# Performance work log

Hardware: AMD Instinct MI355X
Metric: run time of the kernel (lower is better)

## Reference

```python
import jax, jax.numpy as jnp
import numpy as np

T, B, IN, H = 512, 64, 1024, 1024

def setup_inputs() -> dict:
    key = jax.random.key(0)
    ks = jax.random.split(key, 7)
    X = jax.random.normal(ks[0], (T, B, IN), dtype=jnp.float32)
    h0 = jax.random.normal(ks[1], (B, H), dtype=jnp.float32)
    c0 = jax.random.normal(ks[2], (B, H), dtype=jnp.float32)
    mask = jax.random.randint(ks[3], (T, B), 0, 2, dtype=jnp.int32)
    # orthogonal-ish init approximated with scaled normal (math is identical at runtime)
    W_x_ifoc = jax.random.normal(ks[4], (4 * H, IN), dtype=jnp.float32) / np.sqrt(IN)
    W_h_ifoc = jax.random.normal(ks[5], (4 * H, H), dtype=jnp.float32) / np.sqrt(H)
    b_ifoc = jnp.zeros((4 * H,), dtype=jnp.float32)
    return {"X": X, "h0": h0, "c0": c0, "mask": mask,
            "W_x_ifoc": W_x_ifoc, "W_h_ifoc": W_h_ifoc, "b_ifoc": b_ifoc}

def reference(X, h0, c0, mask, W_x_ifoc, W_h_ifoc, b_ifoc):
    Hd = h0.shape[-1]
    # precompute input projection for all timesteps: [T, B, 4H]
    X4 = jnp.einsum('tbi,gi->tbg', X, W_x_ifoc) + b_ifoc
    m_f = mask.astype(X.dtype)[..., None]  # [T, B, 1]

    def step(carry, inp):
        pre_h, pre_c = carry
        x4, m = inp
        # NOTE: recurrent matmul is applied to the CELL state (non-standard)
        pre = x4 + pre_c @ W_h_ifoc.T  # [B, 4H]
        i, f, o, g = jnp.split(pre, 4, axis=-1)
        i = jax.nn.sigmoid(i)
        f = jax.nn.sigmoid(f)
        o = jax.nn.sigmoid(o)
        c = f * pre_c + i * jnp.tanh(g)
        h = o * jnp.tanh(c)
        h = h * m + pre_h * (1 - m)
        c = c * m + pre_c * (1 - m)
        return (h, c), h

    (h_last, c_last), hiddens = jax.lax.scan(step, (h0, c0), (X4, m_f))
    return hiddens, h_last, c_last
```

## Files before the change

kernel.cpp:

```cpp
#include <hip/hip_runtime.h>
#include <cstdint>
#include <cstddef>

#define T_STEPS 512
#define BATCH   64
#define HD      1024
#define BH      (BATCH * HD)
#define NBLK    256
#define NSG     4
#define BSG     16
#define JBLK    16

using half8   = __attribute__((ext_vector_type(8))) _Float16;
using half4   = __attribute__((ext_vector_type(4))) _Float16;
using floatx4 = __attribute__((ext_vector_type(4))) float;
using float4v = __attribute__((ext_vector_type(4))) float;
using u64     = unsigned long long;

__device__ __forceinline__ float sigmoidf_(float x) { return 1.0f / (1.0f + __expf(-x)); }

__device__ __forceinline__ half8 cvt_h8(float4v a, float4v b) {
    half8 r;
    r[0] = (_Float16)a[0]; r[1] = (_Float16)a[1];
    r[2] = (_Float16)a[2]; r[3] = (_Float16)a[3];
    r[4] = (_Float16)b[0]; r[5] = (_Float16)b[1];
    r[6] = (_Float16)b[2]; r[7] = (_Float16)b[3];
    return r;
}

__device__ __forceinline__ void st_sc1_b64(_Float16* p, u64 v) {
    asm volatile("global_store_dwordx2 %0, %1, off sc0 sc1"
                 :: "v"(p), "v"(v) : "memory");
}

__device__ __forceinline__ u64 pack_lo16(unsigned a, unsigned b, unsigned c, unsigned d) {
    return (u64)(a & 0xffffu) | ((u64)(b & 0xffffu) << 16)
         | ((u64)(c & 0xffffu) << 32) | ((u64)(d & 0xffffu) << 48);
}
__device__ __forceinline__ u64 pack_hi16(unsigned a, unsigned b, unsigned c, unsigned d) {
    return (u64)(a >> 16) | ((u64)(b >> 16) << 16)
         | ((u64)(c >> 16) << 32) | ((u64)(d >> 16) << 48);
}

static const size_t BAR_GRP_OFF  = 0;
static const size_t BAR_ROOT_OFF = 20480;
static const size_t CH_OFF  = 24576;
static const size_t CL_OFF  = CH_OFF + (size_t)2 * BH * 2;
static const size_t WX_OFF  = 1u << 20;
static const size_t WHH_OFF = WX_OFF  + (size_t)8 * 1024 * 1024;
static const size_t WHL_OFF = WHH_OFF + (size_t)8 * 1024 * 1024;
static const size_t XH_OFF  = WHL_OFF + (size_t)8 * 1024 * 1024;
static const size_t X4_OFF  = XH_OFF;
static const size_t TIER_A2_WS = X4_OFF + (size_t)32768 * 4096 * 2;
static const size_t TIER_A_WS  = XH_OFF + (size_t)T_STEPS * BH * 2;
static const size_t TIER_B_WS  = XH_OFF;

__global__ void prep_zero(int* bar) {
    int i = blockIdx.x * 256 + threadIdx.x;
    if (i < 6144) bar[i] = 0;
}

__global__ void prep_w(const float* __restrict__ Wx, const float* __restrict__ Wh,
                       _Float16* __restrict__ wx16,
                       _Float16* __restrict__ whh, _Float16* __restrict__ whl) {
    int i = blockIdx.x * 256 + threadIdx.x;
    if (i < 4 * HD * HD) {
        wx16[i] = (_Float16)Wx[i];
        float w = Wh[i];
        _Float16 h = (_Float16)w;
        whh[i] = h;
        whl[i] = (_Float16)(w - (float)h);
    }
}

__global__ void prep_x(const float* __restrict__ X, _Float16* __restrict__ xh) {
    size_t i = (size_t)blockIdx.x * 256 + threadIdx.x;
    if (i < (size_t)T_STEPS * BH) xh[i] = (_Float16)X[i];
}

__global__ __launch_bounds__(256) void x4_gemm(
    const float* __restrict__ X,
    const _Float16* __restrict__ wx16,
    _Float16* __restrict__ x4)
{
    __shared__ _Float16 sA[128][40];
    __shared__ _Float16 sB[128][40];

    const int tid  = threadIdx.x;
    const int wave = tid >> 6;
    const int lane = tid & 63;
    const int m0 = blockIdx.x * 128, n0 = blockIdx.y * 128;
    const int wm = (wave & 1) * 64,  wn = (wave >> 1) * 64;
    const int fm = lane & 15, q = lane >> 4;

    floatx4 acc[4][4];
    #pragma unroll
    for (int i = 0; i < 4; i++)
        #pragma unroll
        for (int j = 0; j < 4; j++)
            acc[i][j] = (floatx4){0.f, 0.f, 0.f, 0.f};

    for (int k0 = 0; k0 < 1024; k0 += 32) {
        {
            const int kq = (tid & 7) * 4;
            const int rb = tid >> 3;
            #pragma unroll
            for (int it = 0; it < 4; it++) {
                int row = rb + it * 32;
                float4v v = *(const float4v*)(X + (size_t)(m0 + row) * 1024 + k0 + kq);
                half4 h; h[0] = (_Float16)v[0]; h[1] = (_Float16)v[1];
                h[2] = (_Float16)v[2]; h[3] = (_Float16)v[3];
                *(half4*)&sA[row][kq] = h;
            }
        }
        {
            const int half = tid & 1;
            const int row  = tid >> 1;
            const _Float16* src = wx16 + (size_t)(n0 + row) * 1024 + k0 + half * 16;
            *(half8*)&sB[row][half * 16]     = *(const half8*)(src);
            *(half8*)&sB[row][half * 16 + 8] = *(const half8*)(src + 8);
        }
        __syncthreads();

        half8 af[4], bf[4];
        #pragma unroll
        for (int i = 0; i < 4; i++) af[i] = *(const half8*)&sA[wm + 16 * i + fm][q * 8];
        #pragma unroll
        for (int j = 0; j < 4; j++) bf[j] = *(const half8*)&sB[wn + 16 * j + fm][q * 8];
        #pragma unroll
        for (int i = 0; i < 4; i++)
            #pragma unroll
            for (int j = 0; j < 4; j++)
                acc[i][j] = __builtin_amdgcn_mfma_f32_16x16x32_f16(af[i], bf[j], acc[i][j], 0, 0, 0);
        __syncthreads();
    }

    #pragma unroll
    for (int i = 0; i < 4; i++)
        #pragma unroll
        for (int j = 0; j < 4; j++)
            #pragma unroll
            for (int r = 0; r < 4; r++) {
                int row = m0 + wm + 16 * i + q * 4 + r;
                int col = n0 + wn + 16 * j + fm;
                x4[(size_t)row * 4096 + col] = (_Float16)acc[i][j][r];
            }
}

__device__ __forceinline__ void grid_bar(int* grp, int* root, int slot) {
    __syncthreads();
    if (threadIdx.x == 0) {
        int g = blockIdx.x >> 5;
        int v = __hip_atomic_fetch_add(&grp[slot * 8 + g], 1,
                                       __ATOMIC_ACQ_REL, __HIP_MEMORY_SCOPE_AGENT);
        if (v == 31)
            __hip_atomic_fetch_add(&root[slot], 1,
                                   __ATOMIC_ACQ_REL, __HIP_MEMORY_SCOPE_AGENT);
        while (__hip_atomic_load(&root[slot], __ATOMIC_RELAXED,
                                 __HIP_MEMORY_SCOPE_AGENT) < 8)
            __builtin_amdgcn_s_sleep(2);
        (void)__hip_atomic_load(&root[slot], __ATOMIC_ACQUIRE,
                                __HIP_MEMORY_SCOPE_AGENT);
    }
    __syncthreads();
}

__device__ __forceinline__ void gbar(int* grp, int* root, int& bcnt) {
    asm volatile("s_waitcnt vmcnt(0)" ::: "memory");
    __syncthreads();
    bcnt++;
    if (threadIdx.x == 0) {
        int v = __hip_atomic_fetch_add(grp, 1, __ATOMIC_RELAXED, __HIP_MEMORY_SCOPE_AGENT);
        if (v == 8 * bcnt - 1)
            __hip_atomic_fetch_add(root, 1, __ATOMIC_RELAXED, __HIP_MEMORY_SCOPE_AGENT);
        while (__hip_atomic_load(root, __ATOMIC_RELAXED, __HIP_MEMORY_SCOPE_AGENT) < 8 * bcnt)
            __builtin_amdgcn_s_sleep(2);
    }
    __syncthreads();
}

__global__ __launch_bounds__(512, 1) void lstm_persist3(
    const _Float16* __restrict__ x4,
    const float* __restrict__ h0, const float* __restrict__ c0,
    const float* __restrict__ bias, const int* __restrict__ mask,
    const _Float16* __restrict__ whh, const _Float16* __restrict__ whl,
    _Float16* __restrict__ chg, _Float16* __restrict__ clg,
    int* __restrict__ bar,
    float* __restrict__ out)
{
    __shared__ float s_pre[8][4][16][18];
    __shared__ float s_h[256], s_c[256];

    const int tid  = threadIdx.x;
    const int wave = tid >> 6;
    const int lane = tid & 63;
    const int sg   = blockIdx.x >> 6;
    const int lb   = blockIdx.x & 63;
    const int b0   = sg * BSG;
    const int j0   = lb * JBLK;

    int* grp  = bar + (sg * 9 + (lb >> 3)) * 64;
    int* root = bar + (sg * 9 + 8) * 64;
    int  bcnt = 0;

    const int nn    = lane & 15;
    const int q     = lane >> 4;
    const int kbase = wave * 128 + q * 8;
    const int arow  = lane & 15;

    half8 wh_[4][4], wl_[4][4];
    #pragma unroll
    for (int g = 0; g < 4; g++) {
        const size_t wr = (size_t)(g * HD + j0 + nn) * HD + kbase;
        #pragma unroll
        for (int k = 0; k < 4; k++) {
            wh_[g][k] = *(const half8*)(whh + wr + k * 32);
            wl_[g][k] = *(const half8*)(whl + wr + k * 32);
        }
    }

    float biasr[4] = {0.f, 0.f, 0.f, 0.f};
    if (tid < 256) {
        int bl = tid >> 4, n = tid & 15;
        int b = b0 + bl, j = j0 + n;
        float cv = c0[b * HD + j];
        s_c[tid] = cv;
        s_h[tid] = h0[b * HD + j];
        #pragma unroll
        for (int g = 0; g < 4; g++) biasr[g] = bias[g * HD + j];

        _Float16 chi = (_Float16)cv;
        _Float16 clo = (_Float16)(cv - (float)chi);
        unsigned pk = (unsigned)__builtin_bit_cast(unsigned short, chi)
                    | ((unsigned)__builtin_bit_cast(unsigned short, clo) << 16);
        unsigned p1 = __shfl_down(pk, 1);
        unsigned p2 = __shfl_down(pk, 2);
        unsigned p3 = __shfl_down(pk, 3);
        if ((n & 3) == 0) {
            st_sc1_b64(chg + b * HD + j0 + (n & ~3), pack_lo16(pk, p1, p2, p3));
            st_sc1_b64(clg + b * HD + j0 + (n & ~3), pack_hi16(pk, p1, p2, p3));
        }
    }
    gbar(grp, root, bcnt);

    for (int t = 0; t < T_STEPS; t++) {
        const int cur = t & 1;

        float xg[4] = {0.f, 0.f, 0.f, 0.f};
        int   mv    = 0;
        if (tid < 256) {
            int b = b0 + (tid >> 4), j = j0 + (tid & 15);
            #pragma unroll
            for (int g = 0; g < 4; g++)
                xg[g] = (float)x4[((size_t)t * BATCH + b) * 4096 + g * HD + j];
            mv = mask[t * BATCH + b];
        }

        const _Float16* chp = chg + (size_t)cur * BH + (size_t)(b0 + arow) * HD + kbase;
        const _Float16* clp = clg + (size_t)cur * BH + (size_t)(b0 + arow) * HD + kbase;

        half8 a0, a1, a2, a3, l0, l1, l2, l3;
        asm volatile(
            "global_load_dwordx4 %0, %8, off sc0 sc1\n\t"
            "global_load_dwordx4 %1, %8, off offset:64 sc0 sc1\n\t"
            "global_load_dwordx4 %2, %8, off offset:128 sc0 sc1\n\t"
            "global_load_dwordx4 %3, %8, off offset:192 sc0 sc1\n\t"
            "global_load_dwordx4 %4, %9, off sc0 sc1\n\t"
            "global_load_dwordx4 %5, %9, off offset:64 sc0 sc1\n\t"
            "global_load_dwordx4 %6, %9, off offset:128 sc0 sc1\n\t"
            "global_load_dwordx4 %7, %9, off offset:192 sc0 sc1\n\t"
            "s_waitcnt vmcnt(0)"
            : "=&v"(a0), "=&v"(a1), "=&v"(a2), "=&v"(a3),
              "=&v"(l0), "=&v"(l1), "=&v"(l2), "=&v"(l3)
            : "v"(chp), "v"(clp)
            : "memory");

        floatx4 acc[4];
        #pragma unroll
        for (int g = 0; g < 4; g++) acc[g] = (floatx4){0.f, 0.f, 0.f, 0.f};
        #pragma unroll
        for (int g = 0; g < 4; g++) {
            floatx4 t0 = acc[g];
            t0 = __builtin_amdgcn_mfma_f32_16x16x32_f16(a0, wh_[g][0], t0, 0, 0, 0);
            t0 = __builtin_amdgcn_mfma_f32_16x16x32_f16(l0, wh_[g][0], t0, 0, 0, 0);
            t0 = __builtin_amdgcn_mfma_f32_16x16x32_f16(a0, wl_[g][0], t0, 0, 0, 0);
            t0 = __builtin_amdgcn_mfma_f32_16x16x32_f16(a1, wh_[g][1], t0, 0, 0, 0);
            t0 = __builtin_amdgcn_mfma_f32_16x16x32_f16(l1, wh_[g][1], t0, 0, 0, 0);
            t0 = __builtin_amdgcn_mfma_f32_16x16x32_f16(a1, wl_[g][1], t0, 0, 0, 0);
            t0 = __builtin_amdgcn_mfma_f32_16x16x32_f16(a2, wh_[g][2], t0, 0, 0, 0);
            t0 = __builtin_amdgcn_mfma_f32_16x16x32_f16(l2, wh_[g][2], t0, 0, 0, 0);
            t0 = __builtin_amdgcn_mfma_f32_16x16x32_f16(a2, wl_[g][2], t0, 0, 0, 0);
            t0 = __builtin_amdgcn_mfma_f32_16x16x32_f16(a3, wh_[g][3], t0, 0, 0, 0);
            t0 = __builtin_amdgcn_mfma_f32_16x16x32_f16(l3, wh_[g][3], t0, 0, 0, 0);
            t0 = __builtin_amdgcn_mfma_f32_16x16x32_f16(a3, wl_[g][3], t0, 0, 0, 0);
            acc[g] = t0;
        }

        #pragma unroll
        for (int g = 0; g < 4; g++) {
            s_pre[wave][g][q * 4 + 0][nn] = acc[g][0];
            s_pre[wave][g][q * 4 + 1][nn] = acc[g][1];
            s_pre[wave][g][q * 4 + 2][nn] = acc[g][2];
            s_pre[wave][g][q * 4 + 3][nn] = acc[g][3];
        }
        __syncthreads();

        if (tid < 256) {
            int bl = tid >> 4, n = tid & 15;
            int b = b0 + bl, j = j0 + n;

            float pg[4];
            #pragma unroll
            for (int g = 0; g < 4; g++) {
                float s = xg[g] + biasr[g];
                #pragma unroll
                for (int kh = 0; kh < 8; kh++)
                    s += s_pre[kh][g][bl][n];
                pg[g] = s;
            }

            float c_old = s_c[tid];
            float i_g = sigmoidf_(pg[0]);
            float f_g = sigmoidf_(pg[1]);
            float o_g = sigmoidf_(pg[2]);
            float g_g = tanhf(pg[3]);
            float c_new = f_g * c_old + i_g * g_g;
            float h_new = o_g * tanhf(c_new);

            float h_out = mv ? h_new : s_h[tid];
            float c_out = mv ? c_new : c_old;
            s_h[tid] = h_out;
            s_c[tid] = c_out;

            out[(size_t)t * BH + (size_t)b * HD + j] = h_out;

            _Float16 chi = (_Float16)c_out;
            _Float16 clo = (_Float16)(c_out - (float)chi);
            unsigned pk = (unsigned)__builtin_bit_cast(unsigned short, chi)
                        | ((unsigned)__builtin_bit_cast(unsigned short, clo) << 16);
            unsigned p1 = __shfl_down(pk, 1);
            unsigned p2 = __shfl_down(pk, 2);
            unsigned p3 = __shfl_down(pk, 3);
            if ((n & 3) == 0) {
                int nxt = cur ^ 1;
                st_sc1_b64(chg + (size_t)nxt * BH + (size_t)b * HD + j0 + (n & ~3),
                           pack_lo16(pk, p1, p2, p3));
                st_sc1_b64(clg + (size_t)nxt * BH + (size_t)b * HD + j0 + (n & ~3),
                           pack_hi16(pk, p1, p2, p3));
            }

            if (t == T_STEPS - 1) {
                size_t tail = (size_t)T_STEPS * BH;
                out[tail + (size_t)b * HD + j]      = h_out;
                out[tail + BH + (size_t)b * HD + j] = c_out;
            }
        }
        gbar(grp, root, bcnt);
    }
}

template<bool XF16>
__global__ __launch_bounds__(1024, 4) void lstm_persist(
    const float* __restrict__ X, const _Float16* __restrict__ xh,
    const float* __restrict__ h0, const float* __restrict__ c0,
    const float* __restrict__ bias, const int* __restrict__ mask,
    const _Float16* __restrict__ wx16, const _Float16* __restrict__ whh,
    const _Float16* __restrict__ whl,
    _Float16* __restrict__ chg, _Float16* __restrict__ clg,
    int* __restrict__ barg, int* __restrict__ barr,
    float* __restrict__ out)
{
    __shared__ _Float16 s_wh[16 * 1032];
    __shared__ float    s_pre[16][16][17];
    __shared__ float    s_h[256], s_c[256];

    const int tid  = threadIdx.x;
    const int wave = tid >> 6;
    const int lane = tid & 63;
    const int j0   = blockIdx.x * 4;

    for (int idx = tid; idx < 2048; idx += 1024) {
        int n  = idx >> 7;
        int kk = (idx & 127) << 3;
        int r  = (n >> 2) * HD + j0 + (n & 3);
        *(half8*)&s_wh[n * 1032 + kk] = *(const half8*)(whh + (size_t)r * HD + kk);
    }

    float biasr[4] = {0.f, 0.f, 0.f, 0.f};
    if (tid < 256) {
        int b = tid >> 2, jj = tid & 3, j = j0 + jj;
        float cv = c0[b * HD + j];
        s_c[tid] = cv;
        s_h[tid] = h0[b * HD + j];
        _Float16 hi = (_Float16)cv;
        chg[b * HD + j] = hi;
        clg[b * HD + j] = (_Float16)(cv - (float)hi);
        #pragma unroll
        for (int g = 0; g < 4; g++) biasr[g] = bias[g * HD + j];
    }
    grid_bar(barg, barr, 0);

    const int mt    = wave & 3;
    const int kh    = wave >> 2;
    const int arow  = mt * 16 + (lane & 15);
    const int nn    = lane & 15;
    const int q     = lane >> 4;
    const int kbase = kh * 256 + q * 8;
    const int wrow  = (nn >> 2) * HD + j0 + (nn & 3);

    const _Float16* wxp = wx16 + (size_t)wrow * HD + kbase;
    const _Float16* wlp = whl  + (size_t)wrow * HD + kbase;
    const _Float16* whp = (const _Float16*)&s_wh[nn * 1032 + kbase];

    for (int t = 0; t < T_STEPS; t++) {
        const int cur = t & 1;
        const _Float16* chp = chg + (size_t)cur * BH + (size_t)arow * HD + kbase;
        const _Float16* clp = clg + (size_t)cur * BH + (size_t)arow * HD + kbase;

        floatx4 acc = {0.f, 0.f, 0.f, 0.f};

        if (XF16) {
            const _Float16* xp = xh + (size_t)t * BH + (size_t)arow * HD + kbase;
            #pragma unroll 4
            for (int k = 0; k < 256; k += 32) {
                half8 av = *(const half8*)(xp + k);
                half8 bv = *(const half8*)(wxp + k);
                acc = __builtin_amdgcn_mfma_f32_16x16x32_f16(av, bv, acc, 0, 0, 0);
            }
        } else {
            const float* xp = X + (size_t)t * BH + (size_t)arow * HD + kbase;
            #pragma unroll 4
            for (int k = 0; k < 256; k += 32) {
                float4v x0 = *(const float4v*)(xp + k);
                float4v x1 = *(const float4v*)(xp + k + 4);
                half8 av = cvt_h8(x0, x1);
                half8 bv = *(const half8*)(wxp + k);
                acc = __builtin_amdgcn_mfma_f32_16x16x32_f16(av, bv, acc, 0, 0, 0);
            }
        }

        #pragma unroll 4
        for (int k = 0; k < 256; k += 32) {
            half8 ah = *(const half8*)(chp + k);
            half8 al = *(const half8*)(clp + k);
            half8 bh = *(const half8*)(whp + k);
            half8 bl = *(const half8*)(wlp + k);
            acc = __builtin_amdgcn_mfma_f32_16x16x32_f16(ah, bh, acc, 0, 0, 0);
            acc = __builtin_amdgcn_mfma_f32_16x16x32_f16(al, bh, acc, 0, 0, 0);
            acc = __builtin_amdgcn_mfma_f32_16x16x32_f16(ah, bl, acc, 0, 0, 0);
        }

        s_pre[wave][q * 4 + 0][nn] = acc[0];
        s_pre[wave][q * 4 + 1][nn] = acc[1];
        s_pre[wave][q * 4 + 2][nn] = acc[2];
        s_pre[wave][q * 4 + 3][nn] = acc[3];
        __syncthreads();

        if (tid < 256) {
            int b = tid >> 2, jj = tid & 3, j = j0 + jj;
            int m = b & 15, mtt = b >> 4;

            float pg[4];
            #pragma unroll
            for (int g = 0; g < 4; g++) {
                float s = 0.f;
                #pragma unroll
                for (int kk = 0; kk < 4; kk++)
                    s += s_pre[kk * 4 + mtt][m][g * 4 + jj];
                pg[g] = s + biasr[g];
            }

            float c_old = s_c[tid];
            float i_g = sigmoidf_(pg[0]);
            float f_g = sigmoidf_(pg[1]);
            float o_g = sigmoidf_(pg[2]);
            float g_g = tanhf(pg[3]);
            float c_new = f_g * c_old + i_g * g_g;
            float h_new = o_g * tanhf(c_new);

            int mv = mask[t * BATCH + b];
            float h_out = mv ? h_new : s_h[tid];
            float c_out = mv ? c_new : c_old;
            s_h[tid] = h_out;
            s_c[tid] = c_out;

            int nxt = cur ^ 1;
            _Float16 hi = (_Float16)c_out;
            chg[(size_t)nxt * BH + b * HD + j] = hi;
            clg[(size_t)nxt * BH + b * HD + j] = (_Float16)(c_out - (float)hi);
            out[(size_t)t * BH + b * HD + j] = h_out;

            if (t == T_STEPS - 1) {
                size_t tail = (size_t)T_STEPS * BH;
                out[tail + b * HD + j]      = h_out;
                out[tail + BH + b * HD + j] = c_out;
            }
        }
        grid_bar(barg, barr, t + 1);
    }
}

__global__ void init_c_fb(const float* __restrict__ c0, float* __restrict__ cf,
                          _Float16* __restrict__ ch, _Float16* __restrict__ cl) {
    int i = blockIdx.x * 256 + threadIdx.x;
    if (i < BH) {
        float v = c0[i];
        cf[i] = v;
        _Float16 h = (_Float16)v;
        ch[i] = h;
        cl[i] = (_Float16)(v - (float)h);
    }
}

__global__ __launch_bounds__(1024) void lstm_step_fb(
    const float* __restrict__ X, const float* __restrict__ h0,
    const float* __restrict__ Wx, const float* __restrict__ Wh,
    const float* __restrict__ bias, const int* __restrict__ mask,
    float* __restrict__ cf, _Float16* __restrict__ chbuf, _Float16* __restrict__ clbuf,
    float* __restrict__ out, int t)
{
    __shared__ float lds_pre[4][64][16];
    const int tid = threadIdx.x, wave = tid >> 6, lane = tid & 63;
    const int g = wave & 3, mt = wave >> 2, j0 = blockIdx.x * 16;
    const int cur = t & 1;
    const float* cf_prev = cf + (size_t)cur * BH;
    const _Float16* ch_prev = chbuf + (size_t)cur * BH;
    const _Float16* cl_prev = clbuf + (size_t)cur * BH;
    float* cf_next = cf + (size_t)(cur ^ 1) * BH;
    _Float16* ch_next = chbuf + (size_t)(cur ^ 1) * BH;
    _Float16* cl_next = clbuf + (size_t)(cur ^ 1) * BH;
    const int arow = mt * 16 + (lane & 15);
    const int brow = g * HD + j0 + (lane & 15);
    const int koff = (lane >> 4) * 8;
    floatx4 acc = {0.f, 0.f, 0.f, 0.f};
    {
        const float* xp = X + (size_t)t * BH + (size_t)arow * HD + koff;
        const float* wp = Wx + (size_t)brow * HD + koff;
        #pragma unroll 4
        for (int k = 0; k < HD; k += 32) {
            float4v x0 = *(const float4v*)(xp + k);
            float4v x1 = *(const float4v*)(xp + k + 4);
            float4v w0 = *(const float4v*)(wp + k);
            float4v w1 = *(const float4v*)(wp + k + 4);
            acc = __builtin_amdgcn_mfma_f32_16x16x32_f16(cvt_h8(x0, x1), cvt_h8(w0, w1), acc, 0, 0, 0);
        }
    }
    {
        const _Float16* chp = ch_prev + (size_t)arow * HD + koff;
        const _Float16* clp = cl_prev + (size_t)arow * HD + koff;
        const float* whp = Wh + (size_t)brow * HD + koff;
        #pragma unroll 4
        for (int k = 0; k < HD; k += 32) {
            half8 ah = *(const half8*)(chp + k);
            half8 al = *(const half8*)(clp + k);
            float4v w0 = *(const float4v*)(whp + k);
            float4v w1 = *(const float4v*)(whp + k + 4);
            half8 bh = cvt_h8(w0, w1);
            float4v r0, r1;
            r0[0] = w0[0] - (float)bh[0]; r0[1] = w0[1] - (float)bh[1];
            r0[2] = w0[2] - (float)bh[2]; r0[3] = w0[3] - (float)bh[3];
            r1[0] = w1[0] - (float)bh[4]; r1[1] = w1[1] - (float)bh[5];
            r1[2] = w1[2] - (float)bh[6]; r1[3] = w1[3] - (float)bh[7];
            half8 bl = cvt_h8(r0, r1);
            acc = __builtin_amdgcn_mfma_f32_16x16x32_f16(ah, bh, acc, 0, 0, 0);
            acc = __builtin_amdgcn_mfma_f32_16x16x32_f16(al, bh, acc, 0, 0, 0);
            acc = __builtin_amdgcn_mfma_f32_16x16x32_f16(ah, bl, acc, 0, 0, 0);
        }
    }
    {
        const int qq = lane >> 4, col = lane & 15;
        lds_pre[g][mt * 16 + qq * 4 + 0][col] = acc[0];
        lds_pre[g][mt * 16 + qq * 4 + 1][col] = acc[1];
        lds_pre[g][mt * 16 + qq * 4 + 2][col] = acc[2];
        lds_pre[g][mt * 16 + qq * 4 + 3][col] = acc[3];
    }
    __syncthreads();
    {
        const int bl2 = tid >> 4, n = tid & 15, j = j0 + n;
        float pg[4];
        #pragma unroll
        for (int gg = 0; gg < 4; gg++) pg[gg] = lds_pre[gg][bl2][n] + bias[gg * HD + j];
        float c_old = cf_prev[bl2 * HD + j];
        float i_g = sigmoidf_(pg[0]), f_g = sigmoidf_(pg[1]);
        float o_g = sigmoidf_(pg[2]), g_g = tanhf(pg[3]);
        float c_new = f_g * c_old + i_g * g_g;
        float h_new = o_g * tanhf(c_new);
        int mv = mask[t * BATCH + bl2];
        float h_prev = (t == 0) ? h0[bl2 * HD + j] : out[(size_t)(t - 1) * BH + bl2 * HD + j];
        float h_out = mv ? h_new : h_prev;
        float c_out = mv ? c_new : c_old;
        cf_next[bl2 * HD + j] = c_out;
        _Float16 hh = (_Float16)c_out;
        ch_next[bl2 * HD + j] = hh;
        cl_next[bl2 * HD + j] = (_Float16)(c_out - (float)hh);
        out[(size_t)t * BH + bl2 * HD + j] = h_out;
        if (t == T_STEPS - 1) {
            size_t tail = (size_t)T_STEPS * BH;
            out[tail + bl2 * HD + j] = h_out;
            out[tail + BH + bl2 * HD + j] = c_out;
        }
    }
}

extern "C" void kernel_launch(void* const* d_in, const int* in_sizes, int n_in,
                              void* d_out, int out_size, void* d_ws, size_t ws_size,
                              hipStream_t stream) {
    const float* X    = (const float*)d_in[0];
    const float* h0   = (const float*)d_in[1];
    const float* c0   = (const float*)d_in[2];
    const int*   mask = (const int*)  d_in[3];
    const float* Wx   = (const float*)d_in[4];
    const float* Wh   = (const float*)d_in[5];
    const float* bias = (const float*)d_in[6];
    float* out = (float*)d_out;
    char* ws = (char*)d_ws;

    if (ws_size >= TIER_B_WS) {
        int*      barg = (int*)(ws + BAR_GRP_OFF);
        int*      barr = (int*)(ws + BAR_ROOT_OFF);
        _Float16* chg  = (_Float16*)(ws + CH_OFF);
        _Float16* clg  = (_Float16*)(ws + CL_OFF);
        _Float16* wx16 = (_Float16*)(ws + WX_OFF);
        _Float16* whh  = (_Float16*)(ws + WHH_OFF);
        _Float16* whl  = (_Float16*)(ws + WHL_OFF);

        prep_zero<<<dim3(24), dim3(256), 0, stream>>>(barg);
        prep_w<<<dim3(16384), dim3(256), 0, stream>>>(Wx, Wh, wx16, whh, whl);

        if (ws_size >= TIER_A2_WS) {
            _Float16* x4 = (_Float16*)(ws + X4_OFF);
            x4_gemm<<<dim3(256, 32), dim3(256), 0, stream>>>(X, wx16, x4);
            void* args[] = {
                (void*)&x4, (void*)&h0, (void*)&c0, (void*)&bias, (void*)&mask,
                (void*)&whh, (void*)&whl, (void*)&chg, (void*)&clg,
                (void*)&barg, (void*)&out
            };
            hipLaunchCooperativeKernel((const void*)&lstm_persist3,
                                       dim3(NBLK), dim3(512), args, 0, stream);
        } else {
            _Float16* xh = (_Float16*)(ws + XH_OFF);
            const bool tierA = ws_size >= TIER_A_WS;
            if (tierA)
                prep_x<<<dim3(131072), dim3(256), 0, stream>>>(X, xh);
            void* args[] = {
                (void*)&X, (void*)&xh, (void*)&h0, (void*)&c0, (void*)&bias,
                (void*)&mask, (void*)&wx16, (void*)&whh, (void*)&whl,
                (void*)&chg, (void*)&clg, (void*)&barg, (void*)&barr, (void*)&out
            };
            if (tierA)
                hipLaunchCooperativeKernel((const void*)&lstm_persist<true>,
                                           dim3(NBLK), dim3(1024), args, 0, stream);
            else
                hipLaunchCooperativeKernel((const void*)&lstm_persist<false>,
                                           dim3(NBLK), dim3(1024), args, 0, stream);
        }
    } else {
        float*    cf = (float*)ws;
        _Float16* ch = (_Float16*)(ws + 524288);
        _Float16* cl = (_Float16*)(ws + 786432);
        init_c_fb<<<dim3((BH + 255) / 256), dim3(256), 0, stream>>>(c0, cf, ch, cl);
        for (int t = 0; t < T_STEPS; t++)
            lstm_step_fb<<<dim3(64), dim3(1024), 0, stream>>>(
                X, h0, Wx, Wh, bias, mask, cf, ch, cl, out, t);
    }
}
```

Measured before the change: 3.909 ms.

## Replace hierarchical grid barrier with per-block step flags and prefetch inputs

Replaces the two-level atomic counter barrier with per-block monotonically increasing step flags. Each wave polls the 64 producer flags of its batch subgroup with a wave-wide vote before loading the shared cell state. The hidden-state output store and the next step's x4/mask loads are moved after the flag publish so they overlap with waiting rather than delaying the release. This removes the serial group-to-root atomic chain and lets blocks advance once their own producers finish, but relies on relaxed atomics plus vmcnt waits for ordering and adds many flag loads per wave.

```diff
diff --git a/kernel.cpp b/kernel.cpp
--- a/kernel.cpp
+++ b/kernel.cpp
@@ -165,21 +165,7 @@
     __syncthreads();
 }
 
-__device__ __forceinline__ void gbar(int* grp, int* root, int& bcnt) {
-    asm volatile("s_waitcnt vmcnt(0)" ::: "memory");
-    __syncthreads();
-    bcnt++;
-    if (threadIdx.x == 0) {
-        int v = __hip_atomic_fetch_add(grp, 1, __ATOMIC_RELAXED, __HIP_MEMORY_SCOPE_AGENT);
-        if (v == 8 * bcnt - 1)
-            __hip_atomic_fetch_add(root, 1, __ATOMIC_RELAXED, __HIP_MEMORY_SCOPE_AGENT);
-        while (__hip_atomic_load(root, __ATOMIC_RELAXED, __HIP_MEMORY_SCOPE_AGENT) < 8 * bcnt)
-            __builtin_amdgcn_s_sleep(2);
-    }
-    __syncthreads();
-}
-
-__global__ __launch_bounds__(512, 1) void lstm_persist3(
+__global__ __launch_bounds__(512, 1) void lstm_persist4(
     const _Float16* __restrict__ x4,
     const float* __restrict__ h0, const float* __restrict__ c0,
     const float* __restrict__ bias, const int* __restrict__ mask,
@@ -199,9 +185,8 @@
     const int b0   = sg * BSG;
     const int j0   = lb * JBLK;
 
-    int* grp  = bar + (sg * 9 + (lb >> 3)) * 64;
-    int* root = bar + (sg * 9 + 8) * 64;
-    int  bcnt = 0;
+    int*       myflag = bar + (((sg << 6) | lb) << 4);
+    const int* pflag  = bar + (((sg << 6) | (wave << 3) | (lane & 7)) << 4);
 
     const int nn    = lane & 15;
     const int q     = lane >> 4;
@@ -220,6 +205,8 @@
     }
 
     float biasr[4] = {0.f, 0.f, 0.f, 0.f};
+    float xg[4]    = {0.f, 0.f, 0.f, 0.f};
+    int   mv       = 0;
     if (tid < 256) {
         int bl = tid >> 4, n = tid & 15;
         int b = b0 + bl, j = j0 + n;
@@ -240,20 +227,24 @@
             st_sc1_b64(chg + b * HD + j0 + (n & ~3), pack_lo16(pk, p1, p2, p3));
             st_sc1_b64(clg + b * HD + j0 + (n & ~3), pack_hi16(pk, p1, p2, p3));
         }
-    }
-    gbar(grp, root, bcnt);
+        #pragma unroll
+        for (int g = 0; g < 4; g++)
+            xg[g] = (float)x4[(size_t)b * 4096 + g * HD + j];
+        mv = mask[b];
+        asm volatile("s_waitcnt vmcnt(0)" ::: "memory");
+    }
+    __syncthreads();
+    if (tid == 0)
+        __hip_atomic_store(myflag, 1, __ATOMIC_RELAXED, __HIP_MEMORY_SCOPE_AGENT);
 
     for (int t = 0; t < T_STEPS; t++) {
         const int cur = t & 1;
 
-        float xg[4] = {0.f, 0.f, 0.f, 0.f};
-        int   mv    = 0;
-        if (tid < 256) {
-            int b = b0 + (tid >> 4), j = j0 + (tid & 15);
-            #pragma unroll
-            for (int g = 0; g < 4; g++)
-                xg[g] = (float)x4[((size_t)t * BATCH + b) * 4096 + g * HD + j];
-            mv = mask[t * BATCH + b];
+        const int need = t + 1;
+        int fv = __hip_atomic_load(pflag, __ATOMIC_RELAXED, __HIP_MEMORY_SCOPE_AGENT);
+        while (!__all(fv >= need)) {
+            __builtin_amdgcn_s_sleep(1);
+            fv = __hip_atomic_load(pflag, __ATOMIC_RELAXED, __HIP_MEMORY_SCOPE_AGENT);
         }
 
         const _Float16* chp = chg + (size_t)cur * BH + (size_t)(b0 + arow) * HD + kbase;
@@ -305,6 +296,7 @@
         }
         __syncthreads();
 
+        float h_out = 0.f, c_out = 0.f;
         if (tid < 256) {
             int bl = tid >> 4, n = tid & 15;
             int b = b0 + bl, j = j0 + n;
@@ -327,12 +319,10 @@
             float c_new = f_g * c_old + i_g * g_g;
             float h_new = o_g * tanhf(c_new);
 
-            float h_out = mv ? h_new : s_h[tid];
-            float c_out = mv ? c_new : c_old;
+            h_out = mv ? h_new : s_h[tid];
+            c_out = mv ? c_new : c_old;
             s_h[tid] = h_out;
             s_c[tid] = c_out;
-
-            out[(size_t)t * BH + (size_t)b * HD + j] = h_out;
 
             _Float16 chi = (_Float16)c_out;
             _Float16 clo = (_Float16)(c_out - (float)chi);
@@ -348,14 +338,27 @@
                 st_sc1_b64(clg + (size_t)nxt * BH + (size_t)b * HD + j0 + (n & ~3),
                            pack_hi16(pk, p1, p2, p3));
             }
-
+            asm volatile("s_waitcnt vmcnt(0)" ::: "memory");
+        }
+        __syncthreads();
+        if (tid == 0)
+            __hip_atomic_store(myflag, t + 2, __ATOMIC_RELAXED, __HIP_MEMORY_SCOPE_AGENT);
+
+        if (tid < 256) {
+            int bl = tid >> 4, n = tid & 15;
+            int b = b0 + bl, j = j0 + n;
+            out[(size_t)t * BH + (size_t)b * HD + j] = h_out;
             if (t == T_STEPS - 1) {
                 size_t tail = (size_t)T_STEPS * BH;
                 out[tail + (size_t)b * HD + j]      = h_out;
                 out[tail + BH + (size_t)b * HD + j] = c_out;
             }
-        }
-        gbar(grp, root, bcnt);
+            int tn = (t + 1 < T_STEPS) ? t + 1 : t;
+            #pragma unroll
+            for (int g = 0; g < 4; g++)
+                xg[g] = (float)x4[((size_t)tn * BATCH + b) * 4096 + g * HD + j];
+            mv = mask[tn * BATCH + b];
+        }
     }
 }
 
@@ -635,7 +638,7 @@
                 (void*)&whh, (void*)&whl, (void*)&chg, (void*)&clg,
                 (void*)&barg, (void*)&out
             };
-            hipLaunchCooperativeKernel((const void*)&lstm_persist3,
+            hipLaunchCooperativeKernel((const void*)&lstm_persist4,
                                        dim3(NBLK), dim3(512), args, 0, stream);
         } else {
             _Float16* xh = (_Float16*)(ws + XH_OFF);
```

Result: faster. 3.169 ms (-18.9%).
